# Performance work log

Hardware: AMD Instinct MI355X
Metric: run time of the kernel (lower is better)

Reference implementation:

```python
import jax, jax.numpy as jnp
import numpy as np

N = 50000
E = 800000
CIN = 32
COUT = 64
DIM = 2
KS = 5                      # kernel size per pseudo-coordinate dim
K = KS ** DIM               # 25 kernel weight matrices
DEGREE = 1
S = (DEGREE + 1) ** DIM     # 4 nonzero B-spline basis products per edge


def _spline_basis(pseudo):
    # pseudo: [E, DIM] in [0, 1]; open linear (degree-1) B-splines per dim.
    v = pseudo * (KS - DEGREE)                              # [E, DIM]
    lo = jnp.floor(v)
    frac = v - lo                                           # [E, DIM]
    lo = jnp.clip(lo.astype(jnp.int32), 0, KS - 2)          # guard p == 1
    bits = (jnp.arange(S)[:, None] >> jnp.arange(DIM)[None, :]) & 1   # [S, DIM]
    # tensor-product basis values: [E, S]
    b = jnp.where(bits[None].astype(bool), frac[:, None, :], 1.0 - frac[:, None, :])
    basis = jnp.prod(b, axis=-1)
    offsets = (KS ** jnp.arange(DIM)).astype(jnp.int32)     # flat-index strides
    wi = jnp.sum((lo[:, None, :] + bits[None]) * offsets[None, None, :], axis=-1)  # [E, S]
    return basis, wi


def setup_inputs() -> dict:
    key = jax.random.key(0)
    k1, k2, k3, k4, k5, k6 = jax.random.split(key, 6)
    bound = 1.0 / np.sqrt(CIN * K)
    x = jax.random.normal(k1, (N, CIN), dtype=jnp.float32)
    edge_index = jax.random.randint(k2, (2, E), 0, N, dtype=jnp.int64)
    pseudo = jax.random.uniform(k3, (E, DIM), dtype=jnp.float32)
    weight = jax.random.uniform(k4, (K, CIN, COUT), minval=-bound, maxval=bound, dtype=jnp.float32)
    root = jax.random.uniform(k5, (CIN, COUT), minval=-bound, maxval=bound, dtype=jnp.float32)
    bias = jax.random.uniform(k6, (COUT,), minval=-bound, maxval=bound, dtype=jnp.float32)
    return {"x": x, "edge_index": edge_index, "pseudo": pseudo,
            "weight": weight, "root": root, "bias": bias}


def reference(x, edge_index, pseudo, weight, root, bias):
    n, cin = x.shape
    cout = weight.shape[-1]
    row = edge_index[0]   # destination nodes (scatter target)
    col = edge_index[1]   # source nodes (gather)
    basis, wi = _spline_basis(pseudo)                       # [E, S], [E, S]
    # Transform every node by every kernel weight matrix: [N, K, Cout]
    y = jnp.einsum('ni,kio->nko', x, weight)
    flat = y.reshape(n * K, cout)
    g = flat[col[:, None] * K + wi]                         # [E, S, Cout] gather
    msg = jnp.einsum('es,eso->eo', basis, g)                # [E, Cout]
    out = jax.ops.segment_sum(msg, row, num_segments=n)     # scatter-add to dst
    deg = jax.ops.segment_sum(jnp.ones((row.shape[0],), dtype=x.dtype), row, num_segments=n)
    out = out / jnp.maximum(deg, 1.0)[:, None]              # degree normalization
    out = out + x @ root + bias                             # root transform + bias
    return out
```

## Files before the change

### kernel.cpp

```cpp
#include <hip/hip_runtime.h>

#define N_NODES 50000
#define E_EDGES 800000
#define CIN     32
#define COUT    64
#define NB      16
#define BCAP    54016
#define NCB     196
#define RCAP    4864
#define SCANB   1024
#define NSCANBLK ((N_NODES + SCANB - 1) / SCANB)
#define EPB     8
#define BBLK    ((E_EDGES + EPB * 256 - 1) / (EPB * 256))
#define XCHUNK  (N_NODES * CIN / 4)
#define KPAD    136

typedef __attribute__((ext_vector_type(8))) short s8v;
typedef __attribute__((ext_vector_type(4))) float f4v;
typedef __attribute__((ext_vector_type(4))) unsigned short u4v;

static __device__ inline unsigned short f2bf(float f) {
    __bf16 b = (__bf16)f;
    return __builtin_bit_cast(unsigned short, b);
}
static __device__ inline float bf2f(unsigned short h) {
    unsigned u = ((unsigned)h) << 16;
    return __builtin_bit_cast(float, u);
}
static __device__ inline unsigned f2bf2(float a, float b) {
    return (unsigned)f2bf(a) | ((unsigned)f2bf(b) << 16);
}


__global__ __launch_bounds__(256) void build_recs(
    const float* __restrict__ x, unsigned short* __restrict__ xbf,
    const int* __restrict__ ei, const float* __restrict__ pseudo,
    int* __restrict__ cursor, int* __restrict__ cursR,
    unsigned long long* __restrict__ recs, unsigned* __restrict__ rp)
{
    {
        const int cb = blockIdx.x * 1024;
#pragma unroll
        for (int k = 0; k < 4; ++k) {
            const int i = cb + k * 256 + threadIdx.x;
            if (i < XCHUNK) {
                f4v v = *(const f4v*)(x + (size_t)i * 4);
                union { unsigned u2[2]; u4v v4; } o;
                o.u2[0] = f2bf2(v[0], v[1]);
                o.u2[1] = f2bf2(v[2], v[3]);
                *(u4v*)(xbf + (size_t)i * 4) = o.v4;
            }
        }
    }

    __shared__ int lh[NB];
    __shared__ int lbase[NB];
    __shared__ int lh2[NCB];
    __shared__ int lbase2[NCB];
    if (threadIdx.x < NB) lh[threadIdx.x] = 0;
    if (threadIdx.x < NCB) lh2[threadIdx.x] = 0;
    __syncthreads();

    const int ebase0 = blockIdx.x * (EPB * 256);
    unsigned long long rcache[EPB];
    int pcache[EPB];
    int pcache2[EPB];

#pragma unroll
    for (int i = 0; i < EPB; ++i) {
        const int e = ebase0 + i * 256 + threadIdx.x;
        pcache[i] = -1; pcache2[i] = -1;
        if (e < E_EDGES) {
            const int row = min(max(ei[e], 0), N_NODES - 1);
            const int col = min(max(ei[E_EDGES + e], 0), N_NODES - 1);
            const float v0 = pseudo[2 * e] * 4.0f, v1 = pseudo[2 * e + 1] * 4.0f;
            const float fl0 = floorf(v0), fl1 = floorf(v1);
            const int lo0 = min(max((int)fl0, 0), 3);
            const int lo1 = min(max((int)fl1, 0), 3);
            const int f0q = min((int)((v0 - fl0) * 65536.0f), 65535);
            const int f1q = min((int)((v1 - fl1) * 65536.0f), 65535);
            const int b = lo0 + 4 * lo1;
            rcache[i] = (unsigned long long)row
                      | ((unsigned long long)col << 16)
                      | ((unsigned long long)f0q << 32)
                      | ((unsigned long long)f1q << 48);
            pcache[i]  = b | (atomicAdd(&lh[b], 1) << 8);
            const int cb = row >> 8;
            pcache2[i] = cb | (atomicAdd(&lh2[cb], 1) << 8);
        }
    }
    __syncthreads();

    if (threadIdx.x < NB)
        lbase[threadIdx.x] = atomicAdd(&cursor[threadIdx.x], lh[threadIdx.x]);
    if (threadIdx.x < NCB)
        lbase2[threadIdx.x] = atomicAdd(&cursR[threadIdx.x], lh2[threadIdx.x]);
    __syncthreads();

#pragma unroll
    for (int i = 0; i < EPB; ++i) {
        if (pcache[i] >= 0) {
            const int b = pcache[i] & 0xFF;
            const int idx = min(lbase[b] + (pcache[i] >> 8), BCAP - 1);
            const unsigned recslot = (unsigned)(b * BCAP + idx);
            recs[recslot] = rcache[i];
            const int cb = pcache2[i] & 0xFF;
            const int idx2 = min(lbase2[cb] + (pcache2[i] >> 8), RCAP - 1);
            const unsigned rowlow = (unsigned)(rcache[i] & 0xFF);
            rp[(size_t)cb * RCAP + idx2] = recslot | (rowlow << 20);
        }
    }
}

__global__ __launch_bounds__(256) void deg_hist(
    const unsigned* __restrict__ rp, const int* __restrict__ cursR,
    int* __restrict__ degi)
{
    __shared__ int h[256];
    h[threadIdx.x] = 0;
    __syncthreads();
    const int cb = blockIdx.x;
    const int cnt = min(cursR[cb], RCAP);
    const unsigned* bp = rp + (size_t)cb * RCAP;
    for (int i = threadIdx.x; i < cnt; i += 256)
        atomicAdd(&h[bp[i] >> 20], 1);
    __syncthreads();
    const int row = cb * 256 + threadIdx.x;
    if (row < N_NODES) degi[row] = h[threadIdx.x];
}

__global__ __launch_bounds__(1024) void scan_blocks(
    const int* __restrict__ degi, int* __restrict__ rowstart, int* __restrict__ bsum)
{
    __shared__ int wsum[16];
    __shared__ int woff[16];
    const int tid = threadIdx.x, lane = tid & 63, wid = tid >> 6;
    const int n = blockIdx.x * SCANB + tid;
    const int v = (n < N_NODES) ? degi[n] : 0;
    int val = v;
#pragma unroll
    for (int off = 1; off < 64; off <<= 1) {
        int t = __shfl_up(val, off);
        if (lane >= off) val += t;
    }
    if (lane == 63) wsum[wid] = val;
    __syncthreads();
    if (tid == 0) {
        int a = 0;
#pragma unroll
        for (int w = 0; w < 16; ++w) { woff[w] = a; a += wsum[w]; }
        bsum[blockIdx.x] = a;
    }
    __syncthreads();
    if (n < N_NODES) rowstart[n] = woff[wid] + (val - v);
}

__global__ __launch_bounds__(1024) void scan_finish(
    int* __restrict__ rowstart, const int* __restrict__ bsum)
{
    const int b = blockIdx.x;
    int off = 0;
    for (int i = 0; i < NSCANBLK; ++i)
        off += (i < b) ? bsum[i] : 0;
    const int n = b * SCANB + threadIdx.x;
    if (n < N_NODES) rowstart[n] += off;
    if (b == NSCANBLK - 1 && threadIdx.x == 0)
        rowstart[N_NODES] = off + bsum[NSCANBLK - 1];
}

__global__ __launch_bounds__(256) void rank_write(
    const unsigned* __restrict__ rp, const int* __restrict__ cursR,
    const int* __restrict__ rowstart, int* __restrict__ dpos)
{
    __shared__ int cur[256];
    const int cb = blockIdx.x;
    const int row = cb * 256 + threadIdx.x;
    cur[threadIdx.x] = (row < N_NODES) ? rowstart[row] : 0;
    __syncthreads();
    const int cnt = min(cursR[cb], RCAP);
    const unsigned* bp = rp + (size_t)cb * RCAP;
    for (int i = threadIdx.x; i < cnt; i += 256) {
        const unsigned e = bp[i];
        const int pos = min(atomicAdd(&cur[e >> 20], 1), E_EDGES - 1);
        dpos[e & 0xFFFFF] = pos;
    }
}

__global__ __launch_bounds__(256, 2) void bucket_mfma_seq(
    const unsigned short* __restrict__ xbf, const float* __restrict__ weight,
    const unsigned long long* __restrict__ recs,
    const int* __restrict__ cursor,
    const int* __restrict__ dpos, unsigned short* __restrict__ msg)
{
    __shared__ short XS[4][2048];

    const int lane = threadIdx.x & 63;
    const int wid  = threadIdx.x >> 6;
    const int cell = blockIdx.x & (NB - 1);
    const int wGlob   = (blockIdx.x >> 4) * 4 + wid;
    const int wStride = (gridDim.x >> 4) * 4;
    const int eg = lane >> 2, part = lane & 3;

    const int lo0 = cell & 3, lo1 = cell >> 2;
    const int base = lo0 + 5 * lo1;
    const int offs[4] = {0, 1, 5, 6};
    const int q = lane >> 4;
    const int c = lane & 15;

    s8v bfr[4][4];
#pragma unroll
    for (int s = 0; s < 4; ++s) {
        const float* wp = weight + (size_t)(base + offs[s]) * (CIN * COUT);
#pragma unroll
        for (int nt = 0; nt < 4; ++nt) {
            union { unsigned short u[8]; s8v v; } tmp;
#pragma unroll
            for (int j = 0; j < 8; ++j)
                tmp.u[j] = f2bf(wp[(q * 8 + j) * COUT + nt * 16 + c]);
            bfr[s][nt] = tmp.v;
        }
    }

    short* const swrow = &XS[wid][eg * 128];
    int swoff[4];
#pragma unroll
    for (int s = 0; s < 4; ++s) swoff[s] = ((4 * s + part + eg) & 15) * 8;
    const short* const arrow = &XS[wid][c * 128];
    int aroff[4];
#pragma unroll
    for (int ks = 0; ks < 4; ++ks) aroff[ks] = ((4 * ks + q + c) & 15) * 8;
    const int erlo = eg * 64 + ((part + eg) & 7) * 8;
    const int erhi = eg * 64 + ((part + 4 + eg) & 7) * 8;

    const unsigned long long* brec = recs + (size_t)cell * BCAP;
    const int* bdp = dpos + (size_t)cell * BCAP;
    const int cnt    = min(cursor[cell], BCAP);
    const int ntiles = (cnt + 15) >> 4;

    int t = wGlob;
    unsigned long long rec_c = 0;
    int dp_c  = 0;
    s8v x_c = {};
    if (t < ntiles) {
        const int ri = min(t * 16 + eg, cnt - 1);
        rec_c = brec[ri];
        dp_c  = bdp[ri];
        x_c = *(const s8v*)(xbf + (size_t)((rec_c >> 16) & 0xFFFF) * CIN + part * 8);
    }

    for (; t < ntiles; t += wStride) {
        const int tn = t + wStride;
        unsigned long long rec_n = 0;
        int dp_n  = 0;
        if (tn < ntiles) {
            const int ri = min(tn * 16 + eg, cnt - 1);
            rec_n = brec[ri];
            dp_n  = bdp[ri];
        }

        const bool vcur = (t * 16 + eg) < cnt;
        const float f0 = (float)(int)((rec_c >> 32) & 0xFFFF) * (1.0f / 65536.0f);
        const float f1 = (float)(int)((rec_c >> 48) & 0xFFFF) * (1.0f / 65536.0f);
        const float s0 = (1.0f - f0) * (1.0f - f1);
        const float s1 = f0 * (1.0f - f1);
        const float s2 = (1.0f - f0) * f1;
        const float s3 = f0 * f1;

        {
            union { unsigned short u[8]; s8v v; } xin; xin.v = x_c;
            float xv[8];
#pragma unroll
            for (int j = 0; j < 8; ++j) xv[j] = bf2f(xin.u[j]);
            const float ss[4] = {s0, s1, s2, s3};
#pragma unroll
            for (int s = 0; s < 4; ++s) {
                union { unsigned u2[4]; s8v v; } tmp;
#pragma unroll
                for (int j = 0; j < 8; j += 2)
                    tmp.u2[j >> 1] = f2bf2(ss[s] * xv[j], ss[s] * xv[j + 1]);
                *(s8v*)(swrow + swoff[s]) = tmp.v;
            }
        }
        __builtin_amdgcn_wave_barrier();

        s8v afr[4];
#pragma unroll
        for (int ks = 0; ks < 4; ++ks)
            afr[ks] = *(const s8v*)(arrow + aroff[ks]);
        __builtin_amdgcn_wave_barrier();

        s8v x_n = {};
        if (tn < ntiles)
            x_n = *(const s8v*)(xbf + (size_t)((rec_n >> 16) & 0xFFFF) * CIN + part * 8);

        f4v acc[4];
#pragma unroll
        for (int nt = 0; nt < 4; ++nt) {
            acc[nt] = (f4v){0.f, 0.f, 0.f, 0.f};
#pragma unroll
            for (int ks = 0; ks < 4; ++ks)
                acc[nt] = __builtin_amdgcn_mfma_f32_16x16x32_bf16(
                    afr[ks], bfr[ks][nt], acc[nt], 0, 0, 0);
        }

#pragma unroll
        for (int r = 0; r < 4; ++r) {
            const int m = q * 4 + r;
#pragma unroll
            for (int nt = 0; nt < 4; ++nt) {
                const int chunk = (2 * nt + (c >> 3) + m) & 7;
                XS[wid][m * 64 + chunk * 8 + (c & 7)] = (short)f2bf(acc[nt][r]);
            }
        }
        __builtin_amdgcn_wave_barrier();
        if (vcur) {
            s8v vlo = *(const s8v*)&XS[wid][erlo];
            s8v vhi = *(const s8v*)&XS[wid][erhi];
            unsigned short* dst = msg + (size_t)dp_c * COUT + part * 8;
            *(s8v*)dst = vlo;
            *(s8v*)(dst + 32) = vhi;
        }
        __builtin_amdgcn_wave_barrier();

        rec_c = rec_n; dp_c = dp_n; x_c = x_n;
    }
}

__global__ __launch_bounds__(256) void gather_seq(
    const unsigned short* __restrict__ msg,
    const int* __restrict__ rowstart, const float* __restrict__ x,
    const float* __restrict__ root, const float* __restrict__ bias,
    float* __restrict__ out)
{
    const int wave   = (blockIdx.x * blockDim.x + threadIdx.x) >> 6;
    const int lane   = threadIdx.x & 63;
    const int nwaves = (gridDim.x * blockDim.x) >> 6;
    const int g = lane >> 3;
    const int c = lane & 7;

    float rfr[4][8];
#pragma unroll
    for (int i = 0; i < 4; ++i) {
        const int ii = g * 4 + i;
        *(f4v*)&rfr[i][0] = *(const f4v*)(root + (size_t)ii * COUT + c * 8);
        *(f4v*)&rfr[i][4] = *(const f4v*)(root + (size_t)ii * COUT + c * 8 + 4);
    }
    float bs[8];
    *(f4v*)&bs[0] = *(const f4v*)(bias + c * 8);
    *(f4v*)&bs[4] = *(const f4v*)(bias + c * 8 + 4);

    for (int n = wave; n < N_NODES; n += nwaves) {
        const int s  = rowstart[n];
        const int e2 = rowstart[n + 1];
        float acc[8] = {0.f, 0.f, 0.f, 0.f, 0.f, 0.f, 0.f, 0.f};

        for (int p = s + g; p < e2; p += 8) {
            union { s8v v; unsigned short u[8]; } mv;
            mv.v = *(const s8v*)(msg + (size_t)p * COUT + c * 8);
#pragma unroll
            for (int j = 0; j < 8; ++j)
                acc[j] += bf2f(mv.u[j]);
        }

        const float invd = 1.0f / (float)max(e2 - s, 1);
#pragma unroll
        for (int j = 0; j < 8; ++j) acc[j] *= invd;

        const f4v xv4 = *(const f4v*)(x + (size_t)n * CIN + g * 4);
#pragma unroll
        for (int i = 0; i < 4; ++i) {
            const float xv = xv4[i];
#pragma unroll
            for (int j = 0; j < 8; ++j)
                acc[j] += xv * rfr[i][j];
        }

#pragma unroll
        for (int off = 8; off < 64; off <<= 1) {
#pragma unroll
            for (int j = 0; j < 8; ++j)
                acc[j] += __shfl_xor(acc[j], off);
        }

        if (g == 0) {
            f4v o0, o1;
#pragma unroll
            for (int j = 0; j < 4; ++j) o0[j] = acc[j] + bs[j];
#pragma unroll
            for (int j = 0; j < 4; ++j) o1[j] = acc[4 + j] + bs[4 + j];
            float* op = out + (size_t)n * COUT + c * 8;
            *(f4v*)op = o0;
            *(f4v*)(op + 4) = o1;
        }
    }
}


__global__ __launch_bounds__(256) void count_fb(
    const int* __restrict__ ei, const float* __restrict__ pseudo,
    int* __restrict__ hist, float* __restrict__ deg)
{
    __shared__ int lh[16];
    if (threadIdx.x < 16) lh[threadIdx.x] = 0;
    __syncthreads();
    const int e = blockIdx.x * 256 + threadIdx.x;
    if (e < E_EDGES) {
        int row = min(max(ei[e], 0), N_NODES - 1);
        const float v0 = pseudo[2 * e] * 4.0f, v1 = pseudo[2 * e + 1] * 4.0f;
        const int lo0 = min(max((int)floorf(v0), 0), 3);
        const int lo1 = min(max((int)floorf(v1), 0), 3);
        atomicAdd(&lh[lo0 + 4 * lo1], 1);
        atomicAdd(&deg[row], 1.0f);
    }
    __syncthreads();
    if (threadIdx.x < 16) atomicAdd(&hist[threadIdx.x], lh[threadIdx.x]);
}

__global__ void scan16_fb(const int* __restrict__ hist,
                          int* __restrict__ bstart, int* __restrict__ cursor)
{
    if (threadIdx.x == 0 && blockIdx.x == 0) {
        int acc = 0;
        for (int c = 0; c < 16; ++c) { bstart[c] = acc; cursor[c] = acc; acc += hist[c]; }
    }
}

__global__ __launch_bounds__(256) void scatter_fb(
    const float* __restrict__ pseudo, int* __restrict__ cursor, int* __restrict__ list)
{
    __shared__ int lh[16];
    __shared__ int lbase[16];
    if (threadIdx.x < 16) lh[threadIdx.x] = 0;
    __syncthreads();
    const int e = blockIdx.x * 256 + threadIdx.x;
    int cell = 0, myoff = 0;
    if (e < E_EDGES) {
        const float v0 = pseudo[2 * e] * 4.0f, v1 = pseudo[2 * e + 1] * 4.0f;
        const int lo0 = min(max((int)floorf(v0), 0), 3);
        const int lo1 = min(max((int)floorf(v1), 0), 3);
        cell = lo0 + 4 * lo1;
        myoff = atomicAdd(&lh[cell], 1);
    }
    __syncthreads();
    if (threadIdx.x < 16)
        lbase[threadIdx.x] = atomicAdd(&cursor[threadIdx.x], lh[threadIdx.x]);
    __syncthreads();
    if (e < E_EDGES)
        list[lbase[cell] + myoff] = e;
}

__global__ __launch_bounds__(256, 2) void bucket_mfma_fb(
    const float* __restrict__ x, const int* __restrict__ ei,
    const float* __restrict__ pseudo, const float* __restrict__ weight,
    const int* __restrict__ list, const int* __restrict__ bstart,
    const int* __restrict__ hist, float* __restrict__ out)
{
    __shared__ short XS[4][16 * KPAD];
    const int lane = threadIdx.x & 63;
    const int wid  = threadIdx.x >> 6;
    const int beta = blockIdx.x & 15;
    const int wGlob   = (blockIdx.x >> 4) * 4 + wid;
    const int wStride = (gridDim.x >> 4) * 4;
    const int lo0 = beta & 3, lo1 = beta >> 2;
    const int base = lo0 + 5 * lo1;
    const int offs[4] = {0, 1, 5, 6};
    const int q = lane >> 4, c = lane & 15;

    s8v bfr[4][4];
#pragma unroll
    for (int s = 0; s < 4; ++s) {
        const float* wp = weight + (size_t)(base + offs[s]) * (CIN * COUT);
#pragma unroll
        for (int nt = 0; nt < 4; ++nt) {
            union { unsigned short u[8]; s8v v; } tmp;
#pragma unroll
            for (int j = 0; j < 8; ++j)
                tmp.u[j] = f2bf(wp[(q * 8 + j) * COUT + nt * 16 + c]);
            bfr[s][nt] = tmp.v;
        }
    }
    const int start = bstart[beta], cnt = hist[beta];
    const int ntiles = (cnt + 15) >> 4;

    for (int t = wGlob; t < ntiles; t += wStride) {
        const int ebase = start + t * 16;
        int rowv = 0, colv = 0;
        float b0 = 0.f, b1 = 0.f, b2 = 0.f, b3 = 0.f;
        if (lane < 16 && (t * 16 + lane) < cnt) {
            const int e = list[ebase + lane];
            rowv = min(max(ei[e], 0), N_NODES - 1);
            colv = min(max(ei[E_EDGES + e], 0), N_NODES - 1);
            const float v0 = pseudo[2 * e] * 4.0f, v1 = pseudo[2 * e + 1] * 4.0f;
            const float f0 = v0 - floorf(v0), f1 = v1 - floorf(v1);
            b0 = (1.0f - f0) * (1.0f - f1);
            b1 = f0 * (1.0f - f1);
            b2 = (1.0f - f0) * f1;
            b3 = f0 * f1;
        }
        {
            const int eg = lane >> 2, part = lane & 3;
            const int  gc = __shfl(colv, eg);
            const float ss0 = __shfl(b0, eg), ss1 = __shfl(b1, eg);
            const float ss2 = __shfl(b2, eg), ss3 = __shfl(b3, eg);
            const float ss[4] = {ss0, ss1, ss2, ss3};
            const float* xp = x + (size_t)gc * CIN + part * 8;
            float xv[8];
            *(f4v*)&xv[0] = *(const f4v*)xp;
            *(f4v*)&xv[4] = *(const f4v*)(xp + 4);
            short* dst = &XS[wid][eg * KPAD + part * 8];
#pragma unroll
            for (int s = 0; s < 4; ++s) {
                union { unsigned short u[8]; s8v v; } tmp;
#pragma unroll
                for (int j = 0; j < 8; ++j)
                    tmp.u[j] = f2bf(ss[s] * xv[j]);
                *(s8v*)(dst + s * 32) = tmp.v;
            }
        }
        __builtin_amdgcn_wave_barrier();
        s8v afr[4];
        {
            const short* ap = &XS[wid][c * KPAD + q * 8];
#pragma unroll
            for (int ks = 0; ks < 4; ++ks)
                afr[ks] = *(const s8v*)(ap + ks * 32);
        }
        __builtin_amdgcn_wave_barrier();
        f4v acc[4];
#pragma unroll
        for (int nt = 0; nt < 4; ++nt) {
            acc[nt] = (f4v){0.f, 0.f, 0.f, 0.f};
#pragma unroll
            for (int ks = 0; ks < 4; ++ks)
                acc[nt] = __builtin_amdgcn_mfma_f32_16x16x32_bf16(
                    afr[ks], bfr[ks][nt], acc[nt], 0, 0, 0);
        }
#pragma unroll
        for (int r = 0; r < 4; ++r) {
            const int m = q * 4 + r;
            const int orow = __shfl(rowv, m);
#pragma unroll
            for (int nt = 0; nt < 4; ++nt)
                atomicAdd(&out[(size_t)orow * COUT + nt * 16 + c], acc[nt][r]);
        }
    }
}

__global__ __launch_bounds__(256) void final_fb(
    const float* __restrict__ x, const float* __restrict__ root,
    const float* __restrict__ bias, const float* __restrict__ deg,
    float* __restrict__ out)
{
    const int wave   = (blockIdx.x * blockDim.x + threadIdx.x) >> 6;
    const int lane   = threadIdx.x & 63;
    const int nwaves = (gridDim.x * blockDim.x) >> 6;
    for (int n = wave; n < N_NODES; n += nwaves) {
        const float* xp = x + (size_t)n * CIN;
        float acc = bias[lane];
#pragma unroll
        for (int i = 0; i < CIN; ++i)
            acc += xp[i] * root[i * COUT + lane];
        float dg = deg[n];
        dg = dg > 1.0f ? dg : 1.0f;
        const size_t idx = (size_t)n * COUT + lane;
        out[idx] = out[idx] / dg + acc;
    }
}

extern "C" void kernel_launch(void* const* d_in, const int* in_sizes, int n_in,
                              void* d_out, int out_size, void* d_ws, size_t ws_size,
                              hipStream_t stream) {
    const float* x      = (const float*)d_in[0];
    const int*   ei     = (const int*)d_in[1];
    const float* pseudo = (const float*)d_in[2];
    const float* weight = (const float*)d_in[3];
    const float* root   = (const float*)d_in[4];
    const float* bias   = (const float*)d_in[5];
    float* out = (float*)d_out;

    int* wsI = (int*)d_ws;
    int* cursor16 = wsI;
    int* cursR    = wsI + 32;
    int* degi     = wsI + 256;
    int* rowstart = wsI + 50256;
    int* bsum     = wsI + 100272;
    unsigned long long* recs = (unsigned long long*)((char*)d_ws + 401408);
    unsigned* rp   = (unsigned*)((char*)recs + (size_t)NB * BCAP * 8);
    int* dpos      = (int*)((char*)rp + (size_t)NCB * RCAP * 4);
    unsigned short* xbf = (unsigned short*)((char*)dpos + (size_t)NB * BCAP * 4);
    unsigned short* msg = (unsigned short*)((char*)xbf + (size_t)N_NODES * CIN * 2);
    const size_t needed = 401408 + (size_t)NB * BCAP * 8 + (size_t)NCB * RCAP * 4
                        + (size_t)NB * BCAP * 4 + (size_t)N_NODES * CIN * 2
                        + (size_t)E_EDGES * COUT * 2;

    if (ws_size >= needed) {
        (void)hipMemsetAsync(d_ws, 0, 256 * 4, stream);
        build_recs <<<BBLK, 256, 0, stream>>>(x, xbf, ei, pseudo, cursor16, cursR, recs, rp);
        deg_hist   <<<NCB, 256, 0, stream>>>(rp, cursR, degi);
        scan_blocks<<<NSCANBLK, 1024, 0, stream>>>(degi, rowstart, bsum);
        scan_finish<<<NSCANBLK, 1024, 0, stream>>>(rowstart, bsum);
        rank_write <<<NCB, 256, 0, stream>>>(rp, cursR, rowstart, dpos);
        bucket_mfma_seq<<<16 * 128, 256, 0, stream>>>(
            xbf, weight, recs, cursor16, dpos, msg);
        gather_seq<<<4096, 256, 0, stream>>>(msg, rowstart, x, root, bias, out);
    } else {
        char* w = (char*)d_ws;
        float* degF   = (float*)w;
        int*   histF  = (int*)(w + 200064);
        int*   bstF   = (int*)(w + 200128);
        int*   curF   = (int*)(w + 200192);
        int*   listF  = (int*)(w + 200256);
        const int eblocks = (E_EDGES + 255) / 256;

        (void)hipMemsetAsync(out, 0, sizeof(float) * (size_t)N_NODES * COUT, stream);
        (void)hipMemsetAsync(degF, 0, sizeof(float) * (size_t)N_NODES, stream);
        (void)hipMemsetAsync(histF, 0, 192, stream);

        count_fb      <<<eblocks, 256, 0, stream>>>(ei, pseudo, histF, degF);
        scan16_fb     <<<1, 64, 0, stream>>>(histF, bstF, curF);
        scatter_fb    <<<eblocks, 256, 0, stream>>>(pseudo, curF, listF);
        bucket_mfma_fb<<<16 * 64, 256, 0, stream>>>(x, ei, pseudo, weight, listF,
                                                    bstF, histF, out);
        final_fb      <<<1024, 256, 0, stream>>>(x, root, bias, degF, out);
    }
}
```

Before: 173.2 us.

## Fuse degree histogram, scan and rank into per-bucket kernel with bucket-level scan

Replaces the four-kernel pipeline (degree histogram, two-pass global scan, rank write) with a tiny single-block scan over per-bucket edge counts followed by one per-bucket kernel. That kernel caches the bucket's entries in LDS, builds the per-row histogram, scans it locally, writes rowstart and assigns destination positions. This removes two kernel launches and a second global read of the bucket lists. The cost is a large LDS array per block, which may limit occupancy in that kernel.

```diff
diff --git a/kernel.cpp b/kernel.cpp
--- a/kernel.cpp
+++ b/kernel.cpp
@@ -8,8 +8,6 @@
 #define BCAP    54016
 #define NCB     196
 #define RCAP    4864
-#define SCANB   1024
-#define NSCANBLK ((N_NODES + SCANB - 1) / SCANB)
 #define EPB     8
 #define BBLK    ((E_EDGES + EPB * 256 - 1) / (EPB * 256))
 #define XCHUNK  (N_NODES * CIN / 4)
@@ -112,75 +110,80 @@
     }
 }
 
-__global__ __launch_bounds__(256) void deg_hist(
-    const unsigned* __restrict__ rp, const int* __restrict__ cursR,
-    int* __restrict__ degi)
-{
-    __shared__ int h[256];
-    h[threadIdx.x] = 0;
-    __syncthreads();
-    const int cb = blockIdx.x;
-    const int cnt = min(cursR[cb], RCAP);
-    const unsigned* bp = rp + (size_t)cb * RCAP;
-    for (int i = threadIdx.x; i < cnt; i += 256)
-        atomicAdd(&h[bp[i] >> 20], 1);
-    __syncthreads();
-    const int row = cb * 256 + threadIdx.x;
-    if (row < N_NODES) degi[row] = h[threadIdx.x];
-}
-
-__global__ __launch_bounds__(1024) void scan_blocks(
-    const int* __restrict__ degi, int* __restrict__ rowstart, int* __restrict__ bsum)
-{
-    __shared__ int wsum[16];
-    __shared__ int woff[16];
+__global__ __launch_bounds__(256) void scanR_k(
+    const int* __restrict__ cursR, int* __restrict__ bstartR,
+    int* __restrict__ rowstart)
+{
+    __shared__ int ws[4];
+    __shared__ int wo[4];
     const int tid = threadIdx.x, lane = tid & 63, wid = tid >> 6;
-    const int n = blockIdx.x * SCANB + tid;
-    const int v = (n < N_NODES) ? degi[n] : 0;
+    const int v = (tid < NCB) ? min(cursR[tid], RCAP) : 0;
     int val = v;
 #pragma unroll
     for (int off = 1; off < 64; off <<= 1) {
         int t = __shfl_up(val, off);
         if (lane >= off) val += t;
     }
-    if (lane == 63) wsum[wid] = val;
+    if (lane == 63) ws[wid] = val;
     __syncthreads();
     if (tid == 0) {
         int a = 0;
 #pragma unroll
-        for (int w = 0; w < 16; ++w) { woff[w] = a; a += wsum[w]; }
-        bsum[blockIdx.x] = a;
-    }
-    __syncthreads();
-    if (n < N_NODES) rowstart[n] = woff[wid] + (val - v);
-}
-
-__global__ __launch_bounds__(1024) void scan_finish(
-    int* __restrict__ rowstart, const int* __restrict__ bsum)
-{
-    const int b = blockIdx.x;
-    int off = 0;
-    for (int i = 0; i < NSCANBLK; ++i)
-        off += (i < b) ? bsum[i] : 0;
-    const int n = b * SCANB + threadIdx.x;
-    if (n < N_NODES) rowstart[n] += off;
-    if (b == NSCANBLK - 1 && threadIdx.x == 0)
-        rowstart[N_NODES] = off + bsum[NSCANBLK - 1];
-}
-
-__global__ __launch_bounds__(256) void rank_write(
+        for (int w = 0; w < 4; ++w) { wo[w] = a; a += ws[w]; }
+    }
+    __syncthreads();
+    if (tid < NCB) bstartR[tid] = wo[wid] + val - v;
+    if (tid == 0) rowstart[N_NODES] = wo[3] + ws[3];
+}
+
+__global__ __launch_bounds__(256) void bucket_rank(
     const unsigned* __restrict__ rp, const int* __restrict__ cursR,
-    const int* __restrict__ rowstart, int* __restrict__ dpos)
-{
+    const int* __restrict__ bstartR,
+    int* __restrict__ rowstart, int* __restrict__ dpos)
+{
+    __shared__ unsigned ent[RCAP];
+    __shared__ int h[256];
+    __shared__ int ws[4];
+    __shared__ int wo[4];
     __shared__ int cur[256];
-    const int cb = blockIdx.x;
-    const int row = cb * 256 + threadIdx.x;
-    cur[threadIdx.x] = (row < N_NODES) ? rowstart[row] : 0;
-    __syncthreads();
+    const int cb = blockIdx.x, tid = threadIdx.x;
+    const int lane = tid & 63, wid = tid >> 6;
+    h[tid] = 0;
+    __syncthreads();
+
     const int cnt = min(cursR[cb], RCAP);
     const unsigned* bp = rp + (size_t)cb * RCAP;
-    for (int i = threadIdx.x; i < cnt; i += 256) {
+    for (int i = tid; i < cnt; i += 256) {
         const unsigned e = bp[i];
+        ent[i] = e;
+        atomicAdd(&h[e >> 20], 1);
+    }
+    __syncthreads();
+
+    const int v = h[tid];
+    int val = v;
+#pragma unroll
+    for (int off = 1; off < 64; off <<= 1) {
+        int t = __shfl_up(val, off);
+        if (lane >= off) val += t;
+    }
+    if (lane == 63) ws[wid] = val;
+    __syncthreads();
+    if (tid == 0) {
+        int a = 0;
+#pragma unroll
+        for (int w = 0; w < 4; ++w) { wo[w] = a; a += ws[w]; }
+    }
+    __syncthreads();
+
+    const int rs = bstartR[cb] + wo[wid] + (val - v);
+    const int row = cb * 256 + tid;
+    if (row < N_NODES) rowstart[row] = rs;
+    cur[tid] = rs;
+    __syncthreads();
+
+    for (int i = tid; i < cnt; i += 256) {
+        const unsigned e = ent[i];
         const int pos = min(atomicAdd(&cur[e >> 20], 1), E_EDGES - 1);
         dpos[e & 0xFFFFF] = pos;
     }
@@ -581,9 +584,8 @@
     int* wsI = (int*)d_ws;
     int* cursor16 = wsI;
     int* cursR    = wsI + 32;
-    int* degi     = wsI + 256;
+    int* bstartR  = wsI + 256;
     int* rowstart = wsI + 50256;
-    int* bsum     = wsI + 100272;
     unsigned long long* recs = (unsigned long long*)((char*)d_ws + 401408);
     unsigned* rp   = (unsigned*)((char*)recs + (size_t)NB * BCAP * 8);
     int* dpos      = (int*)((char*)rp + (size_t)NCB * RCAP * 4);
@@ -596,10 +598,8 @@
     if (ws_size >= needed) {
         (void)hipMemsetAsync(d_ws, 0, 256 * 4, stream);
         build_recs <<<BBLK, 256, 0, stream>>>(x, xbf, ei, pseudo, cursor16, cursR, recs, rp);
-        deg_hist   <<<NCB, 256, 0, stream>>>(rp, cursR, degi);
-        scan_blocks<<<NSCANBLK, 1024, 0, stream>>>(degi, rowstart, bsum);
-        scan_finish<<<NSCANBLK, 1024, 0, stream>>>(rowstart, bsum);
-        rank_write <<<NCB, 256, 0, stream>>>(rp, cursR, rowstart, dpos);
+        scanR_k    <<<1, 256, 0, stream>>>(cursR, bstartR, rowstart);
+        bucket_rank<<<NCB, 256, 0, stream>>>(rp, cursR, bstartR, rowstart, dpos);
         bucket_mfma_seq<<<16 * 128, 256, 0, stream>>>(
             xbf, weight, recs, cursor16, dpos, msg);
         gather_seq<<<4096, 256, 0, stream>>>(msg, rowstart, x, root, bias, out);
```

Result: faster. 163.8 us (-5.4%).
